# Optimization experiments

Hardware: AMD Instinct MI355X
Metric: run time of the kernel (lower is better)

## Reference

```python
import jax, jax.numpy as jnp
import numpy as np

# --- constants matching DILConfig ---
N_DIFF = 1000      # num_diffusion_steps
STEPS = 4          # inference_steps
S_MAX = 4          # max_scales
BUDGET = 0.2       # entropy_budget
G0 = 2.0           # guidance_strength
ENT_LO = 0.1       # stability_threshold_low
ENT_HI = 0.5       # stability_threshold_high
B, L, C, H = 16, 1024, 128, 512


def setup_inputs() -> dict:
    key = jax.random.key(0)
    ks = jax.random.split(key, 6)
    y_obs = jax.random.normal(ks[0], (B, L, C), dtype=jnp.float32)
    mask = (jax.random.uniform(ks[1], (B, L, C)) > 0.5).astype(jnp.float32)
    z_init = jax.random.normal(ks[2], (B, L, C), dtype=jnp.float32)
    W1 = jax.random.normal(ks[3], (C, H), dtype=jnp.float32) / np.sqrt(C)
    b1 = jnp.zeros((H,), dtype=jnp.float32)
    W2 = jax.random.normal(ks[4], (H, C), dtype=jnp.float32) / np.sqrt(H)
    b2 = jnp.zeros((C,), dtype=jnp.float32)
    tw = jax.random.normal(ks[5], (H,), dtype=jnp.float32)
    return {"y_obs": y_obs, "mask": mask, "z_init": z_init,
            "W1": W1, "b1": b1, "W2": W2, "b2": b2, "tw": tw}


def _dil_forward(y_obs, mask, z_init, W1, b1, W2, b2, tw):
    # diffusion schedule (linear betas)
    betas = jnp.linspace(1e-4, 0.02, N_DIFF, dtype=jnp.float32)
    ac = jnp.cumprod(1.0 - betas)
    alpha = jnp.sqrt(ac)                     # sqrt_alphas_cumprod
    sigma = jnp.sqrt(1.0 - ac)               # sqrt_one_minus_alphas_cumprod
    lam = jnp.log(alpha) - jnp.log(sigma)    # log-SNR/2

    step = N_DIFF // STEPS
    ks = [N_DIFF - 1 - i * step for i in range(STEPS)]

    def score(z, k):
        # epsilon predictor: channel MLP with scalar time feature
        t_feat = jnp.float32(k) / N_DIFF
        h = jax.nn.gelu(jnp.einsum('blc,ch->blh', z, W1) + b1 + t_feat * tw)
        return jnp.einsum('blh,hc->blc', h, W2) + b2

    z = z_init
    for k in ks:  # fixed small unrolled loop over inference steps
        kp = max(k - step, 0)
        eps = score(z, k)                                   # [B,L,C]
        h_lam = lam[kp] - lam[k]
        base_a = alpha[kp] / alpha[k]
        base_b = sigma[kp] * (jnp.exp(h_lam) - 1.0)

        # entropy map: batch-mean |eps| per pixel
        ent_pix = jnp.mean(jnp.abs(eps), axis=0)            # [L,C]

        # self-guidance on observed entries
        obs_err = (z - y_obs) * mask
        guidance = -obs_err / (jnp.var(obs_err) + 1e-8)     # [B,L,C]

        z_new = z
        # coarse -> fine so finer-scale selected nodes overwrite coarser ones
        for s in range(S_MAX - 1, -1, -1):
            w = 2 ** s
            pooled = ent_pix.reshape(L // w, w, C // w, w).mean(axis=(1, 3))
            Knodes = max(1, int(BUDGET * pooled.size))
            _, idx = jax.lax.top_k(pooled.ravel(), Knodes)
            selg = jnp.zeros((pooled.size,), jnp.float32).at[idx].set(1.0)
            selg = selg.reshape(pooled.shape)
            sel = jnp.repeat(jnp.repeat(selg, w, axis=0), w, axis=1)     # [L,C]
            ent_up = jnp.repeat(jnp.repeat(pooled, w, axis=0), w, axis=1)

            # adaptive solver order from entropy stability thresholds
            order = (1.0 + (ent_up > ENT_LO).astype(jnp.float32)
                         + (ent_up > ENT_HI).astype(jnp.float32))
            corr = (1.0 + (order - 1.0) * 0.5 * h_lam
                        + (order - 1.0) * (order - 2.0) / 6.0 * h_lam ** 2)
            gs = G0 * ent_up / (ent_up + 1.0)               # adaptive guidance

            cand = base_a * z - base_b * (corr * eps) + gs * guidance
            z_new = jnp.where(sel[None, :, :] > 0, cand, z_new)
        z = z_new
    return z


def reference(y_obs, mask, z_init, W1, b1, W2, b2, tw):
    return _dil_forward(y_obs, mask, z_init, W1, b1, W2, b2, tw)
```

## Files before the change

kernel.cpp:

```cpp
#include <hip/hip_runtime.h>
#include <math.h>
#include <stdint.h>

#define L_DIM 1024
#define C_DIM 128
#define H_DIM 512
#define B_DIM 16
#define LC (L_DIM * C_DIM)
#define BLC (B_DIM * LC)

typedef __attribute__((ext_vector_type(8))) short short8;
typedef __attribute__((ext_vector_type(4))) float floatx4;

__device__ __forceinline__ unsigned fordbits(unsigned u) {
    return (u & 0x80000000u) ? ~u : (u | 0x80000000u);
}

__device__ __forceinline__ void split3(float x, unsigned& uh, unsigned& um,
                                       unsigned& ul) {
    uh = __float_as_uint(x);
    const float r1 = x - __uint_as_float(uh & 0xffff0000u);
    um = __float_as_uint(r1);
    const float r2 = r1 - __uint_as_float(um & 0xffff0000u);
    ul = __float_as_uint(r2);
}

__device__ __forceinline__ float gelu_fast(float x) {
    const float g = 0.7978845608028654f * (x + 0.044715f * x * x * x);
    const float e = __expf(2.0f * g);
    const float t = 1.0f - 2.0f / (e + 1.0f);
    return 0.5f * x * (1.0f + t);
}

__global__ __launch_bounds__(256) void wsplit_kernel(
    const float* __restrict__ W1, const float* __restrict__ W2,
    unsigned short* __restrict__ W1h, unsigned short* __restrict__ W1m,
    unsigned short* __restrict__ W1l, unsigned short* __restrict__ W2h,
    unsigned short* __restrict__ W2m, unsigned short* __restrict__ W2l) {
    const int t = blockIdx.x * 256 + threadIdx.x;
    unsigned uh, um, ul;
    if (t < 65536) {
        const int j = t & 7, lane = (t >> 3) & 63, nt = (t >> 9) & 31,
                  kt = (t >> 14) & 3;
        const int k = kt * 32 + (lane >> 4) * 8 + j;
        const int n = nt * 16 + (lane & 15);
        split3(W1[k * 512 + n], uh, um, ul);
        W1h[t] = (unsigned short)(uh >> 16);
        W1m[t] = (unsigned short)(um >> 16);
        W1l[t] = (unsigned short)(ul >> 16);
    } else {
        const int t2 = t - 65536;
        const int j = t2 & 7, lane = (t2 >> 3) & 63, nt = (t2 >> 9) & 7,
                  kt = (t2 >> 12) & 15;
        const int k = kt * 32 + (lane >> 4) * 8 + j;
        const int n = nt * 16 + (lane & 15);
        split3(W2[k * 128 + n], uh, um, ul);
        W2h[t2] = (unsigned short)(uh >> 16);
        W2m[t2] = (unsigned short)(um >> 16);
        W2l[t2] = (unsigned short)(ul >> 16);
    }
}

#define MFMA6(AH, AM, AL, BH, BM, BL, ACC)                                    \
    ACC = __builtin_amdgcn_mfma_f32_16x16x32_bf16(AL, BH, ACC, 0, 0, 0);      \
    ACC = __builtin_amdgcn_mfma_f32_16x16x32_bf16(AM, BM, ACC, 0, 0, 0);      \
    ACC = __builtin_amdgcn_mfma_f32_16x16x32_bf16(AH, BL, ACC, 0, 0, 0);      \
    ACC = __builtin_amdgcn_mfma_f32_16x16x32_bf16(AM, BH, ACC, 0, 0, 0);      \
    ACC = __builtin_amdgcn_mfma_f32_16x16x32_bf16(AH, BM, ACC, 0, 0, 0);      \
    ACC = __builtin_amdgcn_mfma_f32_16x16x32_bf16(AH, BH, ACC, 0, 0, 0);

__device__ __forceinline__ int swz(int row, int col) {
    return row * 128 + ((((col >> 3) ^ (row & 15))) << 3) + (col & 7);
}

template <int UPD>
__global__ __launch_bounds__(512, 4) void mlp_kernel(
    float* __restrict__ z, const float* __restrict__ y,
    const float* __restrict__ mk,
    const unsigned short* __restrict__ W1h, const unsigned short* __restrict__ W1m,
    const unsigned short* __restrict__ W1l, const unsigned short* __restrict__ W2h,
    const unsigned short* __restrict__ W2m, const unsigned short* __restrict__ W2l,
    const float* __restrict__ b1, const float* __restrict__ tw,
    const float* __restrict__ b2, float t_feat,
    float* __restrict__ eps_buf, float* __restrict__ ent,
    const float* __restrict__ cA, const float* __restrict__ cB,
    const float* __restrict__ cG, float* __restrict__ accum) {
    __shared__ unsigned short zA[3][4096];
    __shared__ unsigned short hA[3][4096];
    __shared__ float red1[8], red2[8];
    const int tid = threadIdx.x;
    const int w = tid >> 6, lane = tid & 63;
    const int quad = lane >> 4, m16 = lane & 15;
    const int l0 = blockIdx.x * 2;

    float s1 = 0.f, s2 = 0.f;
#pragma unroll
    for (int e = 0; e < 2; ++e) {
        const int f = tid * 8 + e * 4;
        const int r_ = f >> 7, cb = f & 127;
        const int b = r_ & 15, il = r_ >> 4, l = l0 + il;
        const size_t g = ((size_t)b * 1024 + l) * 128 + cb;
        float4 zv = *(const float4*)(z + g);
        const float4 yv = *(const float4*)(y + g);
        const float4 mv = *(const float4*)(mk + g);
        if (UPD) {
            const float4 ev = *(const float4*)(eps_buf + g);
            const int pix = l * 128 + cb;
            const float4 a4 = *(const float4*)(cA + pix);
            const float4 b4 = *(const float4*)(cB + pix);
            const float4 g4 = *(const float4*)(cG + pix);
            zv.x = a4.x * zv.x - b4.x * ev.x - g4.x * ((zv.x - yv.x) * mv.x);
            zv.y = a4.y * zv.y - b4.y * ev.y - g4.y * ((zv.y - yv.y) * mv.y);
            zv.z = a4.z * zv.z - b4.z * ev.z - g4.z * ((zv.z - yv.z) * mv.z);
            zv.w = a4.w * zv.w - b4.w * ev.w - g4.w * ((zv.w - yv.w) * mv.w);
            *(float4*)(z + g) = zv;
        }
        float oe;
        oe = (zv.x - yv.x) * mv.x; s1 += oe; s2 += oe * oe;
        oe = (zv.y - yv.y) * mv.y; s1 += oe; s2 += oe * oe;
        oe = (zv.z - yv.z) * mv.z; s1 += oe; s2 += oe * oe;
        oe = (zv.w - yv.w) * mv.w; s1 += oe; s2 += oe * oe;

        const int base = swz(r_, cb);
        const float xs[4] = {zv.x, zv.y, zv.z, zv.w};
        ushort4 vh, vm, vl;
        unsigned uh, um, ul;
        split3(xs[0], uh, um, ul); vh.x = uh >> 16; vm.x = um >> 16; vl.x = ul >> 16;
        split3(xs[1], uh, um, ul); vh.y = uh >> 16; vm.y = um >> 16; vl.y = ul >> 16;
        split3(xs[2], uh, um, ul); vh.z = uh >> 16; vm.z = um >> 16; vl.z = ul >> 16;
        split3(xs[3], uh, um, ul); vh.w = uh >> 16; vm.w = um >> 16; vl.w = ul >> 16;
        *(ushort4*)(&zA[0][base]) = vh;
        *(ushort4*)(&zA[1][base]) = vm;
        *(ushort4*)(&zA[2][base]) = vl;
    }
#pragma unroll
    for (int off = 32; off; off >>= 1) {
        s1 += __shfl_down(s1, off);
        s2 += __shfl_down(s2, off);
    }
    if (lane == 0) { red1[w] = s1; red2[w] = s2; }
    __syncthreads();
    if (tid == 0) {
        float a1 = 0.f, a2 = 0.f;
#pragma unroll
        for (int i = 0; i < 8; ++i) { a1 += red1[i]; a2 += red2[i]; }
        atomicAdd(&accum[0], a1);
        atomicAdd(&accum[1], a2);
    }

    floatx4 acc1[8];
#pragma unroll
    for (int i = 0; i < 8; ++i) acc1[i] = (floatx4){0.f, 0.f, 0.f, 0.f};

#pragma unroll
    for (int kt = 0; kt < 4; ++kt) {
        short8 Ah[2], Am[2], Al[2];
#pragma unroll
        for (int il = 0; il < 2; ++il) {
            const int fb = swz(il * 16 + m16, kt * 32 + quad * 8);
            Ah[il] = *(const short8*)(&zA[0][fb]);
            Am[il] = *(const short8*)(&zA[1][fb]);
            Al[il] = *(const short8*)(&zA[2][fb]);
        }
#pragma unroll
        for (int q = 0; q < 4; ++q) {
            const size_t off = ((size_t)(kt * 32 + q * 8 + w) * 64 + lane) * 8;
            const short8 bh = *(const short8*)(W1h + off);
            const short8 bm = *(const short8*)(W1m + off);
            const short8 bl = *(const short8*)(W1l + off);
#pragma unroll
            for (int il = 0; il < 2; ++il) {
                floatx4 a = acc1[q * 2 + il];
                MFMA6(Ah[il], Am[il], Al[il], bh, bm, bl, a);
                acc1[q * 2 + il] = a;
            }
        }
    }

    floatx4 acc2[2];
    acc2[0] = (floatx4){0.f, 0.f, 0.f, 0.f};
    acc2[1] = (floatx4){0.f, 0.f, 0.f, 0.f};

    for (int q = 0; q < 4; ++q) {
        __syncthreads();
        {
            const int colg = q * 128 + w * 16 + m16;
            const float bb = b1[colg] + t_feat * tw[colg];
            const int kcol = w * 16 + m16;
#pragma unroll
            for (int il = 0; il < 2; ++il) {
#pragma unroll
                for (int r = 0; r < 4; ++r) {
                    const float x = gelu_fast(acc1[q * 2 + il][r] + bb);
                    unsigned uh, um, ul;
                    split3(x, uh, um, ul);
                    const int idx = swz(il * 16 + quad * 4 + r, kcol);
                    hA[0][idx] = (unsigned short)(uh >> 16);
                    hA[1][idx] = (unsigned short)(um >> 16);
                    hA[2][idx] = (unsigned short)(ul >> 16);
                }
            }
        }
        __syncthreads();

#pragma unroll
        for (int ktl = 0; ktl < 4; ++ktl) {
            short8 Ah2[2], Am2[2], Al2[2];
#pragma unroll
            for (int il = 0; il < 2; ++il) {
                const int fb = swz(il * 16 + m16, ktl * 32 + quad * 8);
                Ah2[il] = *(const short8*)(&hA[0][fb]);
                Am2[il] = *(const short8*)(&hA[1][fb]);
                Al2[il] = *(const short8*)(&hA[2][fb]);
            }
            const size_t off =
                ((size_t)((q * 4 + ktl) * 8 + w) * 64 + lane) * 8;
            const short8 bh = *(const short8*)(W2h + off);
            const short8 bm = *(const short8*)(W2m + off);
            const short8 bl = *(const short8*)(W2l + off);
#pragma unroll
            for (int il = 0; il < 2; ++il) {
                floatx4 a = acc2[il];
                MFMA6(Ah2[il], Am2[il], Al2[il], bh, bm, bl, a);
                acc2[il] = a;
            }
        }
    }

    {
        const int col = w * 16 + m16;
        const float bb2 = b2[col];
#pragma unroll
        for (int il = 0; il < 2; ++il) {
            float pa = 0.f;
#pragma unroll
            for (int r = 0; r < 4; ++r) {
                const float e = acc2[il][r] + bb2;
                const int b = quad * 4 + r;
                eps_buf[((size_t)b * 1024 + l0 + il) * 128 + col] = e;
                pa += fabsf(e);
            }
            pa += __shfl_xor(pa, 16);
            pa += __shfl_xor(pa, 32);
            if (quad == 0) ent[(l0 + il) * 128 + col] = pa * (1.0f / 16.0f);
        }
    }
}

__device__ __forceinline__ void grid_barrier(unsigned* c, unsigned* r) {
    __syncthreads();
    if (threadIdx.x == 0) {
        __threadfence();
        if (atomicAdd(c, 1u) + 1u == 85u) atomicExch(r, 1u);
        else
            while (atomicAdd(r, 0u) == 0u) __builtin_amdgcn_s_sleep(8);
    }
    __syncthreads();
}

__global__ __launch_bounds__(256, 1) void select_kernel(
    const float* __restrict__ ent, float* __restrict__ p1,
    float* __restrict__ p2, float* __restrict__ p3,
    unsigned* __restrict__ ghist, unsigned* __restrict__ ctr,
    unsigned* __restrict__ rel, unsigned* __restrict__ gprefix,
    float* __restrict__ cA, float* __restrict__ cB, float* __restrict__ cG,
    const float* __restrict__ accum_si, float base_a, float base_b,
    float h_lam, int si) {
    const int bid = blockIdx.x, t = threadIdx.x;
    const int gid = bid * 256 + t;
    const int slot0 = si * 6;

    for (int i = gid; i < 32768; i += 21760) {
        const int r = i >> 6, c = i & 63;
        float s = 0.f;
#pragma unroll
        for (int ii = 0; ii < 2; ++ii)
#pragma unroll
            for (int jj = 0; jj < 2; ++jj)
                s += ent[((r * 2 + ii) << 7) + c * 2 + jj];
        atomicExch((unsigned*)&p1[i], __float_as_uint(s * 0.25f));
    }
    for (int i = gid; i < 8192; i += 21760) {
        const int r = i >> 5, c = i & 31;
        float s = 0.f;
#pragma unroll
        for (int ii = 0; ii < 4; ++ii)
#pragma unroll
            for (int jj = 0; jj < 4; ++jj)
                s += ent[((r * 4 + ii) << 7) + c * 4 + jj];
        atomicExch((unsigned*)&p2[i], __float_as_uint(s * 0.0625f));
    }
    for (int i = gid; i < 2048; i += 21760) {
        const int r = i >> 4, c = i & 15;
        float s = 0.f;
#pragma unroll
        for (int ii = 0; ii < 8; ++ii)
#pragma unroll
            for (int jj = 0; jj < 8; ++jj)
                s += ent[((r * 8 + ii) << 7) + c * 8 + jj];
        atomicExch((unsigned*)&p3[i], __float_as_uint(s * (1.0f / 64.0f)));
    }
    grid_barrier(&ctr[slot0], &rel[slot0]);

    const float* data;
    int scale, base;
    unsigned K;
    if (bid < 64) { scale = 0; data = ent; base = bid * 2048; K = 26214u; }
    else if (bid < 80) { scale = 1; data = p1; base = (bid - 64) * 2048; K = 6553u; }
    else if (bid < 84) { scale = 2; data = p2; base = (bid - 80) * 2048; K = 1638u; }
    else { scale = 3; data = p3; base = 0; K = 409u; }

    __shared__ unsigned hist[4][256];
    __shared__ unsigned sh[256];
    __shared__ unsigned sh_dig, sh_krem;
    const int wv = t >> 6;
    unsigned prefix = 0u, krem = K;

    for (int p = 0; p < 4; ++p) {
        const int shift = 24 - 8 * p;
        const unsigned hmask = p ? (0xFFFFFFFFu << (shift + 8)) : 0u;
#pragma unroll
        for (int i = t; i < 1024; i += 256) ((unsigned*)hist)[i] = 0u;
        __syncthreads();
#pragma unroll
        for (int i = t; i < 2048; i += 256) {
            const unsigned raw = atomicAdd((unsigned*)&data[base + i], 0u);
            const unsigned u = fordbits(raw);
            if ((u & hmask) == (prefix & hmask))
                atomicAdd(&hist[wv][(u >> shift) & 255u], 1u);
        }
        __syncthreads();
        const unsigned c = hist[0][t] + hist[1][t] + hist[2][t] + hist[3][t];
        unsigned* gh = &ghist[((si * 4 + p) * 4 + scale) * 256];
        if (c) atomicAdd(&gh[t], c);
        grid_barrier(&ctr[slot0 + 1 + p], &rel[slot0 + 1 + p]);
        sh[t] = atomicAdd(&gh[t], 0u);
        __syncthreads();
#pragma unroll
        for (int off = 1; off < 256; off <<= 1) {
            const unsigned v = (t + off < 256) ? sh[t + off] : 0u;
            __syncthreads();
            sh[t] += v;
            __syncthreads();
        }
        const unsigned suf = sh[t];
        const unsigned sufn = (t < 255) ? sh[t + 1] : 0u;
        if (suf >= krem && sufn < krem) {
            sh_dig = (unsigned)t;
            sh_krem = krem - sufn;
        }
        __syncthreads();
        prefix |= (sh_dig << shift);
        krem = sh_krem;
        __syncthreads();
    }
    if (t == 0 && base == 0) atomicExch(&gprefix[scale], prefix);
    grid_barrier(&ctr[slot0 + 5], &rel[slot0 + 5]);

    const unsigned t0 = atomicAdd(&gprefix[0], 0u);
    const unsigned t1 = atomicAdd(&gprefix[1], 0u);
    const unsigned t2 = atomicAdd(&gprefix[2], 0u);
    const unsigned t3 = atomicAdd(&gprefix[3], 0u);
    const float mean = accum_si[0] * (1.0f / (float)BLC);
    const float var = accum_si[1] * (1.0f / (float)BLC) - mean * mean;
    const float vinv = 1.0f / (var + 1e-8f);

    for (int i = gid; i < LC; i += 21760) {
        const int l = i >> 7, c = i & 127;
        float ent_v = 0.f;
        bool sel = false;
        const float v0 = ent[i];
        if (fordbits(__float_as_uint(v0)) >= t0) { ent_v = v0; sel = true; }
        else {
            const float v1 = __uint_as_float(atomicAdd(
                (unsigned*)&p1[((l >> 1) << 6) + (c >> 1)], 0u));
            if (fordbits(__float_as_uint(v1)) >= t1) { ent_v = v1; sel = true; }
            else {
                const float v2 = __uint_as_float(atomicAdd(
                    (unsigned*)&p2[((l >> 2) << 5) + (c >> 2)], 0u));
                if (fordbits(__float_as_uint(v2)) >= t2) { ent_v = v2; sel = true; }
                else {
                    const float v3 = __uint_as_float(atomicAdd(
                        (unsigned*)&p3[((l >> 3) << 4) + (c >> 3)], 0u));
                    if (fordbits(__float_as_uint(v3)) >= t3) { ent_v = v3; sel = true; }
                }
            }
        }
        if (sel) {
            float corr;
            if (ent_v > 0.5f)
                corr = 1.0f + h_lam + h_lam * h_lam * (1.0f / 3.0f);
            else if (ent_v > 0.1f)
                corr = 1.0f + 0.5f * h_lam;
            else
                corr = 1.0f;
            cA[i] = base_a;
            cB[i] = base_b * corr;
            cG[i] = (2.0f * ent_v / (ent_v + 1.0f)) * vinv;
        } else {
            cA[i] = 1.0f;
            cB[i] = 0.f;
            cG[i] = 0.f;
        }
    }
}

__global__ __launch_bounds__(256) void update_kernel(
    float* __restrict__ z, const float* __restrict__ y,
    const float* __restrict__ mk, const float* __restrict__ eps,
    const float* __restrict__ cA, const float* __restrict__ cB,
    const float* __restrict__ cG) {
    const int idx = blockIdx.x * 256 + threadIdx.x;
    const int p = idx & (LC - 1);
    const float zi = z[idx];
    z[idx] = cA[p] * zi - cB[p] * eps[idx] - cG[p] * ((zi - y[idx]) * mk[idx]);
}

extern "C" void kernel_launch(void* const* d_in, const int* in_sizes, int n_in,
                              void* d_out, int out_size, void* d_ws,
                              size_t ws_size, hipStream_t stream) {
    const float* y_obs = (const float*)d_in[0];
    const float* mask = (const float*)d_in[1];
    const float* z_init = (const float*)d_in[2];
    const float* W1 = (const float*)d_in[3];
    const float* b1 = (const float*)d_in[4];
    const float* W2 = (const float*)d_in[5];
    const float* b2 = (const float*)d_in[6];
    const float* tw = (const float*)d_in[7];
    float* z = (float*)d_out;
    float* ws = (float*)d_ws;

    float* eps = ws;
    float* ent = ws + 2097152;
    float* p1 = ws + 2228224;
    float* p2 = ws + 2260992;
    float* p3 = ws + 2269184;
    float* cA = ws + 2271232;
    float* cB = ws + 2402304;
    float* cG = ws + 2533376;
    unsigned* ghist = (unsigned*)(ws + 2664448);
    unsigned* ctr = (unsigned*)(ws + 2680832);
    unsigned* rel = (unsigned*)(ws + 2680856);
    float* accum = ws + 2680880;
    unsigned* gprefix = (unsigned*)(ws + 2680888);
    unsigned short* W1h = (unsigned short*)(ws + 2680896);
    unsigned short* W1m = (unsigned short*)(ws + 2713664);
    unsigned short* W1l = (unsigned short*)(ws + 2746432);
    unsigned short* W2h = (unsigned short*)(ws + 2779200);
    unsigned short* W2m = (unsigned short*)(ws + 2811968);
    unsigned short* W2l = (unsigned short*)(ws + 2844736);

    float alpha_[1000], sigma_[1000], lam_[1000];
    {
        float ac = 1.0f;
        for (int i = 0; i < 1000; ++i) {
            const float beta = 1e-4f + (0.02f - 1e-4f) * ((float)i / 999.0f);
            ac = ac * (1.0f - beta);
            alpha_[i] = sqrtf(ac);
            sigma_[i] = sqrtf(1.0f - ac);
            lam_[i] = logf(alpha_[i]) - logf(sigma_[i]);
        }
    }
    float tf[4], hl[4], ba[4], bb[4];
    for (int si = 0; si < 4; ++si) {
        const int k = 999 - si * 250;
        const int kp = (k - 250 > 0) ? (k - 250) : 0;
        tf[si] = (float)k / 1000.0f;
        hl[si] = lam_[kp] - lam_[k];
        ba[si] = alpha_[kp] / alpha_[k];
        bb[si] = sigma_[kp] * (expf(hl[si]) - 1.0f);
    }

    hipMemcpyAsync(z, z_init, sizeof(float) * BLC, hipMemcpyDeviceToDevice,
                   stream);
    hipMemsetAsync(ghist, 0, (16384 + 24 + 24 + 8 + 4) * sizeof(unsigned),
                   stream);
    wsplit_kernel<<<512, 256, 0, stream>>>(W1, W2, W1h, W1m, W1l, W2h, W2m,
                                           W2l);

    for (int si = 0; si < 4; ++si) {
        if (si == 0) {
            mlp_kernel<0><<<512, 512, 0, stream>>>(
                z, y_obs, mask, W1h, W1m, W1l, W2h, W2m, W2l, b1, tw, b2,
                tf[0], eps, ent, cA, cB, cG, accum);
        } else {
            mlp_kernel<1><<<512, 512, 0, stream>>>(
                z, y_obs, mask, W1h, W1m, W1l, W2h, W2m, W2l, b1, tw, b2,
                tf[si], eps, ent, cA, cB, cG, accum + 2 * si);
        }
        select_kernel<<<85, 256, 0, stream>>>(
            ent, p1, p2, p3, ghist, ctr, rel, gprefix, cA, cB, cG,
            accum + 2 * si, ba[si], bb[si], hl[si], si);
    }
    update_kernel<<<8192, 256, 0, stream>>>(z, y_obs, mask, eps, cA, cB, cG);
}
```

Before: 411.0 us.

## Replace grid-barrier select kernel with pools, threshold, and coefficient kernels

The single 85-block select kernel used software grid barriers and atomic loads for its multi-pass radix top-k. It is split into three launches. The first computes the pooled maps and a 14-bit-prefix histogram of the full-resolution entropy. The second runs one block per scale, keeping coarse-scale data in registers and gathering full-scale candidates into LDS for the remaining radix passes. The third applies the coefficients and clears the histogram. This removes the spin-wait barriers and atomic reads, but adds kernel launch overhead and puts the full-scale threshold search on a single block.

After: 517.0 us. +25.8%, slower.

```diff
diff --git a/kernel.cpp b/kernel.cpp
--- a/kernel.cpp
+++ b/kernel.cpp
@@ -247,161 +247,303 @@
     }
 }
 
-__device__ __forceinline__ void grid_barrier(unsigned* c, unsigned* r) {
-    __syncthreads();
-    if (threadIdx.x == 0) {
-        __threadfence();
-        if (atomicAdd(c, 1u) + 1u == 85u) atomicExch(r, 1u);
-        else
-            while (atomicAdd(r, 0u) == 0u) __builtin_amdgcn_s_sleep(8);
-    }
-    __syncthreads();
-}
-
-__global__ __launch_bounds__(256, 1) void select_kernel(
+
+__global__ __launch_bounds__(256) void pools_kernel(
     const float* __restrict__ ent, float* __restrict__ p1,
     float* __restrict__ p2, float* __restrict__ p3,
-    unsigned* __restrict__ ghist, unsigned* __restrict__ ctr,
-    unsigned* __restrict__ rel, unsigned* __restrict__ gprefix,
-    float* __restrict__ cA, float* __restrict__ cB, float* __restrict__ cG,
-    const float* __restrict__ accum_si, float base_a, float base_b,
-    float h_lam, int si) {
-    const int bid = blockIdx.x, t = threadIdx.x;
-    const int gid = bid * 256 + t;
-    const int slot0 = si * 6;
-
-    for (int i = gid; i < 32768; i += 21760) {
-        const int r = i >> 6, c = i & 63;
+    unsigned* __restrict__ ghist) {
+    __shared__ unsigned lh[16384];
+    const int tid = threadIdx.x;
+    const int gid = blockIdx.x * 256 + tid;
+    for (int i = tid; i < 16384; i += 256) lh[i] = 0u;
+    __syncthreads();
+
+    {
+        const float2 ev = *(const float2*)(ent + (size_t)gid * 2);
+        atomicAdd(&lh[fordbits(__float_as_uint(ev.x)) >> 18], 1u);
+        atomicAdd(&lh[fordbits(__float_as_uint(ev.y)) >> 18], 1u);
+    }
+    if (gid < 32768) {
+        const int r = gid >> 6, c = gid & 63;
         float s = 0.f;
 #pragma unroll
         for (int ii = 0; ii < 2; ++ii)
 #pragma unroll
             for (int jj = 0; jj < 2; ++jj)
                 s += ent[((r * 2 + ii) << 7) + c * 2 + jj];
-        atomicExch((unsigned*)&p1[i], __float_as_uint(s * 0.25f));
-    }
-    for (int i = gid; i < 8192; i += 21760) {
-        const int r = i >> 5, c = i & 31;
+        p1[gid] = s * 0.25f;
+    }
+    if (gid < 8192) {
+        const int r = gid >> 5, c = gid & 31;
         float s = 0.f;
 #pragma unroll
         for (int ii = 0; ii < 4; ++ii)
 #pragma unroll
             for (int jj = 0; jj < 4; ++jj)
                 s += ent[((r * 4 + ii) << 7) + c * 4 + jj];
-        atomicExch((unsigned*)&p2[i], __float_as_uint(s * 0.0625f));
-    }
-    for (int i = gid; i < 2048; i += 21760) {
-        const int r = i >> 4, c = i & 15;
+        p2[gid] = s * 0.0625f;
+    }
+    if (gid < 2048) {
+        const int r = gid >> 4, c = gid & 15;
         float s = 0.f;
 #pragma unroll
         for (int ii = 0; ii < 8; ++ii)
 #pragma unroll
             for (int jj = 0; jj < 8; ++jj)
                 s += ent[((r * 8 + ii) << 7) + c * 8 + jj];
-        atomicExch((unsigned*)&p3[i], __float_as_uint(s * (1.0f / 64.0f)));
-    }
-    grid_barrier(&ctr[slot0], &rel[slot0]);
-
-    const float* data;
-    int scale, base;
-    unsigned K;
-    if (bid < 64) { scale = 0; data = ent; base = bid * 2048; K = 26214u; }
-    else if (bid < 80) { scale = 1; data = p1; base = (bid - 64) * 2048; K = 6553u; }
-    else if (bid < 84) { scale = 2; data = p2; base = (bid - 80) * 2048; K = 1638u; }
-    else { scale = 3; data = p3; base = 0; K = 409u; }
-
-    __shared__ unsigned hist[4][256];
-    __shared__ unsigned sh[256];
-    __shared__ unsigned sh_dig, sh_krem;
-    const int wv = t >> 6;
+        p3[gid] = s * (1.0f / 64.0f);
+    }
+    __syncthreads();
+    for (int i = tid; i < 16384; i += 256) {
+        const unsigned c = lh[i];
+        if (c) atomicAdd(&ghist[i], c);
+    }
+}
+
+template <int NPT>
+__device__ __forceinline__ void radix_reg(
+    const float* __restrict__ data, unsigned K, unsigned* __restrict__ gout,
+    const int t, const int w8, unsigned (*hrep)[512], unsigned* part,
+    unsigned* sh_d, unsigned* sh_k2) {
+    unsigned v[NPT];
+#pragma unroll
+    for (int i = 0; i < NPT; ++i)
+        v[i] = fordbits(__float_as_uint(data[t + i * 1024]));
     unsigned prefix = 0u, krem = K;
-
+    if (t == 0) { *sh_d = 0u; *sh_k2 = K; }
     for (int p = 0; p < 4; ++p) {
         const int shift = 24 - 8 * p;
         const unsigned hmask = p ? (0xFFFFFFFFu << (shift + 8)) : 0u;
-#pragma unroll
-        for (int i = t; i < 1024; i += 256) ((unsigned*)hist)[i] = 0u;
-        __syncthreads();
-#pragma unroll
-        for (int i = t; i < 2048; i += 256) {
-            const unsigned raw = atomicAdd((unsigned*)&data[base + i], 0u);
-            const unsigned u = fordbits(raw);
-            if ((u & hmask) == (prefix & hmask))
-                atomicAdd(&hist[wv][(u >> shift) & 255u], 1u);
-        }
-        __syncthreads();
-        const unsigned c = hist[0][t] + hist[1][t] + hist[2][t] + hist[3][t];
-        unsigned* gh = &ghist[((si * 4 + p) * 4 + scale) * 256];
-        if (c) atomicAdd(&gh[t], c);
-        grid_barrier(&ctr[slot0 + 1 + p], &rel[slot0 + 1 + p]);
-        sh[t] = atomicAdd(&gh[t], 0u);
-        __syncthreads();
-#pragma unroll
+        for (int i = t; i < 4096; i += 1024) ((unsigned*)hrep)[i] = 0u;
+        __syncthreads();
+#pragma unroll
+        for (int i = 0; i < NPT; ++i)
+            if ((v[i] & hmask) == (prefix & hmask))
+                atomicAdd(&hrep[w8][(v[i] >> shift) & 255u], 1u);
+        __syncthreads();
+        if (t < 256) {
+            unsigned s = 0;
+#pragma unroll
+            for (int r = 0; r < 8; ++r) s += hrep[r][t];
+            part[t] = s;
+        }
+        __syncthreads();
         for (int off = 1; off < 256; off <<= 1) {
-            const unsigned v = (t + off < 256) ? sh[t + off] : 0u;
+            unsigned vv = 0u;
+            if (t < 256) vv = (t + off < 256) ? part[t + off] : 0u;
             __syncthreads();
-            sh[t] += v;
+            if (t < 256) part[t] += vv;
             __syncthreads();
         }
-        const unsigned suf = sh[t];
-        const unsigned sufn = (t < 255) ? sh[t + 1] : 0u;
-        if (suf >= krem && sufn < krem) {
-            sh_dig = (unsigned)t;
-            sh_krem = krem - sufn;
-        }
-        __syncthreads();
-        prefix |= (sh_dig << shift);
-        krem = sh_krem;
-        __syncthreads();
-    }
-    if (t == 0 && base == 0) atomicExch(&gprefix[scale], prefix);
-    grid_barrier(&ctr[slot0 + 5], &rel[slot0 + 5]);
-
-    const unsigned t0 = atomicAdd(&gprefix[0], 0u);
-    const unsigned t1 = atomicAdd(&gprefix[1], 0u);
-    const unsigned t2 = atomicAdd(&gprefix[2], 0u);
-    const unsigned t3 = atomicAdd(&gprefix[3], 0u);
+        if (t < 256) {
+            const unsigned suf = part[t];
+            const unsigned sufn = (t < 255) ? part[t + 1] : 0u;
+            if (suf >= krem && sufn < krem) {
+                *sh_d = (unsigned)t;
+                *sh_k2 = krem - sufn;
+            }
+        }
+        __syncthreads();
+        prefix |= (*sh_d) << shift;
+        krem = *sh_k2;
+        __syncthreads();
+    }
+    if (t == 0) *gout = prefix;
+}
+
+#define CAND_CAP 12288
+__global__ __launch_bounds__(1024, 1) void thresh_kernel(
+    const float* __restrict__ ent, const float* __restrict__ p1,
+    const float* __restrict__ p2, const float* __restrict__ p3,
+    const unsigned* __restrict__ ghist, unsigned* __restrict__ gprefix) {
+    const int scale = blockIdx.x, t = threadIdx.x;
+    __shared__ unsigned part[1024];
+    __shared__ unsigned hrep[8][512];
+    __shared__ unsigned cand[CAND_CAP];
+    __shared__ unsigned sh_b, sh_krem, sh_cnt, sh_d, sh_k2;
+    const int w8 = (t >> 6) & 7;
+
+    if (scale > 0) {
+        if (scale == 1)
+            radix_reg<32>(p1, 6553u, &gprefix[1], t, w8, hrep, part, &sh_d, &sh_k2);
+        else if (scale == 2)
+            radix_reg<8>(p2, 1638u, &gprefix[2], t, w8, hrep, part, &sh_d, &sh_k2);
+        else
+            radix_reg<2>(p3, 409u, &gprefix[3], t, w8, hrep, part, &sh_d, &sh_k2);
+        return;
+    }
+
+    const unsigned K = 26214u;
+    if (t == 0) { sh_b = 0u; sh_krem = 1u; sh_cnt = 0u; sh_d = 0u; sh_k2 = 1u; }
+
+    {
+        unsigned s = 0;
+        const uint4* h4 = (const uint4*)(ghist + t * 16);
+#pragma unroll
+        for (int j = 0; j < 4; ++j) {
+            const uint4 x = h4[j];
+            s += x.x + x.y + x.z + x.w;
+        }
+        part[t] = s;
+    }
+    __syncthreads();
+    for (int off = 1; off < 1024; off <<= 1) {
+        const unsigned v = (t + off < 1024) ? part[t + off] : 0u;
+        __syncthreads();
+        part[t] += v;
+        __syncthreads();
+    }
+    {
+        const unsigned suf = part[t];
+        const unsigned sufn = (t < 1023) ? part[t + 1] : 0u;
+        if (suf >= K && sufn < K) {
+            unsigned run = sufn;
+            for (int b = 15; b >= 0; --b) {
+                const unsigned hb = ghist[t * 16 + b];
+                run += hb;
+                if (run >= K) {
+                    sh_b = (unsigned)(t * 16 + b);
+                    sh_krem = K - (run - hb);
+                    break;
+                }
+            }
+        }
+    }
+    __syncthreads();
+    const unsigned b14 = sh_b;
+    unsigned krem = sh_krem;
+
+    for (int i = t; i < 131072; i += 1024) {
+        const unsigned u = fordbits(__float_as_uint(ent[i]));
+        if ((u >> 18) == b14) {
+            const unsigned p = atomicAdd(&sh_cnt, 1u);
+            if (p < CAND_CAP) cand[p] = u;
+        }
+    }
+    __syncthreads();
+    const unsigned cnt = sh_cnt;
+    const bool inlds = (cnt <= CAND_CAP);
+
+    for (int i = t; i < 4096; i += 1024) ((unsigned*)hrep)[i] = 0u;
+    __syncthreads();
+    if (inlds) {
+        for (unsigned i = t; i < cnt; i += 1024)
+            atomicAdd(&hrep[w8][(cand[i] >> 9) & 511u], 1u);
+    } else {
+        for (int i = t; i < 131072; i += 1024) {
+            const unsigned u = fordbits(__float_as_uint(ent[i]));
+            if ((u >> 18) == b14) atomicAdd(&hrep[w8][(u >> 9) & 511u], 1u);
+        }
+    }
+    __syncthreads();
+    if (t < 512) {
+        unsigned s = 0;
+#pragma unroll
+        for (int r = 0; r < 8; ++r) s += hrep[r][t];
+        part[t] = s;
+    }
+    __syncthreads();
+    for (int off = 1; off < 512; off <<= 1) {
+        unsigned v = 0u;
+        if (t < 512) v = (t + off < 512) ? part[t + off] : 0u;
+        __syncthreads();
+        if (t < 512) part[t] += v;
+        __syncthreads();
+    }
+    if (t < 512) {
+        const unsigned suf = part[t];
+        const unsigned sufn = (t < 511) ? part[t + 1] : 0u;
+        if (suf >= krem && sufn < krem) { sh_d = (unsigned)t; sh_k2 = krem - sufn; }
+    }
+    __syncthreads();
+    const unsigned dA = sh_d;
+    krem = sh_k2;
+    __syncthreads();
+
+    for (int i = t; i < 4096; i += 1024) ((unsigned*)hrep)[i] = 0u;
+    __syncthreads();
+    if (inlds) {
+        for (unsigned i = t; i < cnt; i += 1024) {
+            const unsigned c = cand[i];
+            if (((c >> 9) & 511u) == dA) atomicAdd(&hrep[w8][c & 511u], 1u);
+        }
+    } else {
+        for (int i = t; i < 131072; i += 1024) {
+            const unsigned u = fordbits(__float_as_uint(ent[i]));
+            if ((u >> 18) == b14 && ((u >> 9) & 511u) == dA)
+                atomicAdd(&hrep[w8][u & 511u], 1u);
+        }
+    }
+    __syncthreads();
+    if (t < 512) {
+        unsigned s = 0;
+#pragma unroll
+        for (int r = 0; r < 8; ++r) s += hrep[r][t];
+        part[t] = s;
+    }
+    __syncthreads();
+    for (int off = 1; off < 512; off <<= 1) {
+        unsigned v = 0u;
+        if (t < 512) v = (t + off < 512) ? part[t + off] : 0u;
+        __syncthreads();
+        if (t < 512) part[t] += v;
+        __syncthreads();
+    }
+    if (t < 512) {
+        const unsigned suf = part[t];
+        const unsigned sufn = (t < 511) ? part[t + 1] : 0u;
+        if (suf >= krem && sufn < krem)
+            gprefix[0] = (b14 << 18) | (dA << 9) | (unsigned)t;
+    }
+}
+
+__global__ __launch_bounds__(256) void coeff_kernel(
+    const float* __restrict__ ent, const float* __restrict__ p1,
+    const float* __restrict__ p2, const float* __restrict__ p3,
+    const unsigned* __restrict__ gprefix, const float* __restrict__ accum_si,
+    float* __restrict__ cA, float* __restrict__ cB, float* __restrict__ cG,
+    unsigned* __restrict__ ghist, float base_a, float base_b, float h_lam) {
+    const int i = blockIdx.x * 256 + threadIdx.x;
+    if (i < 16384) ghist[i] = 0u;
+
+    const unsigned t0 = gprefix[0], t1 = gprefix[1], t2 = gprefix[2],
+                   t3 = gprefix[3];
     const float mean = accum_si[0] * (1.0f / (float)BLC);
     const float var = accum_si[1] * (1.0f / (float)BLC) - mean * mean;
     const float vinv = 1.0f / (var + 1e-8f);
 
-    for (int i = gid; i < LC; i += 21760) {
-        const int l = i >> 7, c = i & 127;
-        float ent_v = 0.f;
-        bool sel = false;
-        const float v0 = ent[i];
-        if (fordbits(__float_as_uint(v0)) >= t0) { ent_v = v0; sel = true; }
+    const int l = i >> 7, c = i & 127;
+    float ent_v = 0.f;
+    bool sel = false;
+    const float v0 = ent[i];
+    if (fordbits(__float_as_uint(v0)) >= t0) { ent_v = v0; sel = true; }
+    else {
+        const float v1 = p1[((l >> 1) << 6) + (c >> 1)];
+        if (fordbits(__float_as_uint(v1)) >= t1) { ent_v = v1; sel = true; }
         else {
-            const float v1 = __uint_as_float(atomicAdd(
-                (unsigned*)&p1[((l >> 1) << 6) + (c >> 1)], 0u));
-            if (fordbits(__float_as_uint(v1)) >= t1) { ent_v = v1; sel = true; }
+            const float v2 = p2[((l >> 2) << 5) + (c >> 2)];
+            if (fordbits(__float_as_uint(v2)) >= t2) { ent_v = v2; sel = true; }
             else {
-                const float v2 = __uint_as_float(atomicAdd(
-                    (unsigned*)&p2[((l >> 2) << 5) + (c >> 2)], 0u));
-                if (fordbits(__float_as_uint(v2)) >= t2) { ent_v = v2; sel = true; }
-                else {
-                    const float v3 = __uint_as_float(atomicAdd(
-                        (unsigned*)&p3[((l >> 3) << 4) + (c >> 3)], 0u));
-                    if (fordbits(__float_as_uint(v3)) >= t3) { ent_v = v3; sel = true; }
-                }
-            }
-        }
-        if (sel) {
-            float corr;
-            if (ent_v > 0.5f)
-                corr = 1.0f + h_lam + h_lam * h_lam * (1.0f / 3.0f);
-            else if (ent_v > 0.1f)
-                corr = 1.0f + 0.5f * h_lam;
-            else
-                corr = 1.0f;
-            cA[i] = base_a;
-            cB[i] = base_b * corr;
-            cG[i] = (2.0f * ent_v / (ent_v + 1.0f)) * vinv;
-        } else {
-            cA[i] = 1.0f;
-            cB[i] = 0.f;
-            cG[i] = 0.f;
-        }
+                const float v3 = p3[((l >> 3) << 4) + (c >> 3)];
+                if (fordbits(__float_as_uint(v3)) >= t3) { ent_v = v3; sel = true; }
+            }
+        }
+    }
+    if (sel) {
+        float corr;
+        if (ent_v > 0.5f)
+            corr = 1.0f + h_lam + h_lam * h_lam * (1.0f / 3.0f);
+        else if (ent_v > 0.1f)
+            corr = 1.0f + 0.5f * h_lam;
+        else
+            corr = 1.0f;
+        cA[i] = base_a;
+        cB[i] = base_b * corr;
+        cG[i] = (2.0f * ent_v / (ent_v + 1.0f)) * vinv;
+    } else {
+        cA[i] = 1.0f;
+        cB[i] = 0.f;
+        cG[i] = 0.f;
     }
 }
 
@@ -438,17 +580,15 @@
     float* cA = ws + 2271232;
     float* cB = ws + 2402304;
     float* cG = ws + 2533376;
-    unsigned* ghist = (unsigned*)(ws + 2664448);
-    unsigned* ctr = (unsigned*)(ws + 2680832);
-    unsigned* rel = (unsigned*)(ws + 2680856);
-    float* accum = ws + 2680880;
-    unsigned* gprefix = (unsigned*)(ws + 2680888);
-    unsigned short* W1h = (unsigned short*)(ws + 2680896);
-    unsigned short* W1m = (unsigned short*)(ws + 2713664);
-    unsigned short* W1l = (unsigned short*)(ws + 2746432);
-    unsigned short* W2h = (unsigned short*)(ws + 2779200);
-    unsigned short* W2m = (unsigned short*)(ws + 2811968);
-    unsigned short* W2l = (unsigned short*)(ws + 2844736);
+    float* accum = ws + 2664448;
+    unsigned* gprefix = (unsigned*)(ws + 2664456);
+    unsigned* ghist = (unsigned*)(ws + 2664460);
+    unsigned short* W1h = (unsigned short*)(ws + 2680844);
+    unsigned short* W1m = (unsigned short*)(ws + 2713612);
+    unsigned short* W1l = (unsigned short*)(ws + 2746380);
+    unsigned short* W2h = (unsigned short*)(ws + 2779148);
+    unsigned short* W2m = (unsigned short*)(ws + 2811916);
+    unsigned short* W2l = (unsigned short*)(ws + 2844684);
 
     float alpha_[1000], sigma_[1000], lam_[1000];
     {
@@ -473,8 +613,7 @@
 
     hipMemcpyAsync(z, z_init, sizeof(float) * BLC, hipMemcpyDeviceToDevice,
                    stream);
-    hipMemsetAsync(ghist, 0, (16384 + 24 + 24 + 8 + 4) * sizeof(unsigned),
-                   stream);
+    hipMemsetAsync(accum, 0, (8 + 4 + 16384) * sizeof(unsigned), stream);
     wsplit_kernel<<<512, 256, 0, stream>>>(W1, W2, W1h, W1m, W1l, W2h, W2m,
                                            W2l);
 
@@ -488,9 +627,11 @@
                 z, y_obs, mask, W1h, W1m, W1l, W2h, W2m, W2l, b1, tw, b2,
                 tf[si], eps, ent, cA, cB, cG, accum + 2 * si);
         }
-        select_kernel<<<85, 256, 0, stream>>>(
-            ent, p1, p2, p3, ghist, ctr, rel, gprefix, cA, cB, cG,
-            accum + 2 * si, ba[si], bb[si], hl[si], si);
+        pools_kernel<<<256, 256, 0, stream>>>(ent, p1, p2, p3, ghist);
+        thresh_kernel<<<4, 1024, 0, stream>>>(ent, p1, p2, p3, ghist, gprefix);
+        coeff_kernel<<<512, 256, 0, stream>>>(ent, p1, p2, p3, gprefix,
+                                              accum + 2 * si, cA, cB, cG,
+                                              ghist, ba[si], bb[si], hl[si]);
     }
     update_kernel<<<8192, 256, 0, stream>>>(z, y_obs, mask, eps, cA, cB, cG);
 }
```
